# Kernel optimization log

Measured on AMD Instinct MI355X. Metric: run time of the kernel, lower is better.

Reference implementation:

```python
import jax, jax.numpy as jnp
import numpy as np

N = 100000      # nodes
E = 1600000     # edges (avg degree 16)
DIN = 128       # in_feats
H = 4           # num_heads
D = 32          # out_feats per head
NEG_SLOPE = 0.2


def setup_inputs() -> dict:
    key = jax.random.key(0)
    k1, k2, k3, k4, k5, k6 = jax.random.split(key, 6)
    feat = jax.random.normal(k1, (N, DIN), dtype=jnp.float32)
    src = jax.random.randint(k2, (E,), 0, N, dtype=jnp.int32)
    dst = jax.random.randint(k3, (E,), 0, N, dtype=jnp.int32)
    # learned params (fc kernel + attention vectors)
    W = jax.random.normal(k4, (DIN, H * D), dtype=jnp.float32) * 0.05
    attn_l = jax.random.normal(k5, (H, D), dtype=jnp.float32) * 0.05
    attn_r = jax.random.normal(k6, (H, D), dtype=jnp.float32) * 0.05
    return {"feat": feat, "src": src, "dst": dst, "W": W,
            "attn_l": attn_l, "attn_r": attn_r}


def reference(feat, src, dst, W, attn_l, attn_r):
    # linear projection: (N, DIN) @ (DIN, H*D) -> (N, H, D)
    h = (feat @ W).reshape(N, H, D)
    # per-node attention half-logits: (N, H)
    el = jnp.einsum("nhd,hd->nh", h, attn_l)
    er = jnp.einsum("nhd,hd->nh", h, attn_r)
    # edge-wise logits e_ij = LeakyReLU(el[src] + er[dst]) : (E, H)
    e = jax.nn.leaky_relu(el[src] + er[dst], negative_slope=NEG_SLOPE)
    # segment softmax over incoming edges of each dst node
    emax = jax.ops.segment_max(e, dst, num_segments=N)          # (N, H)
    emax = jnp.where(jnp.isfinite(emax), emax, 0.0)             # empty segs
    ee = jnp.exp(e - emax[dst])                                 # (E, H)
    denom = jax.ops.segment_sum(ee, dst, num_segments=N)        # (N, H)
    a = ee / denom[dst]                                         # (E, H)
    # weighted message + scatter-sum aggregation: (N, H, D)
    msg = h[src] * a[:, :, None]                                # (E, H, D)
    out = jax.ops.segment_sum(msg, dst, num_segments=N)
    return out
```

## Files before the change

### kernel.cpp

```cpp
#include <hip/hip_runtime.h>
#include <hip/hip_fp16.h>

#define N_NODES 100000
#define N_EDGES 1600000
#define DIN 128
#define NH 4
#define ND 32
#define HD 128
#define NEG_SLOPE 0.2f
#define MROWS 64
#define APAD 136
#define GEMM_BLOCKS ((N_NODES + MROWS - 1) / MROWS)

#define NBUCK 782
#define CHB 8192
#define NHB 196

typedef _Float16 half8_t __attribute__((ext_vector_type(8)));
typedef float f32x4 __attribute__((ext_vector_type(4)));

__device__ __forceinline__ float lrelu(float x) {
    return x > 0.0f ? x : NEG_SLOPE * x;
}

union Pack8  { uint2 u; __half2 h2[2]; };
union Pack16 { uint4 u; __half2 h2[4]; };

__global__ __launch_bounds__(256) void k_wconv(const float* __restrict__ W,
                                               __half* __restrict__ Wt) {
    int i = blockIdx.x * 256 + threadIdx.x;
    int k = i >> 7, c = i & 127;
    Wt[c * DIN + k] = __float2half(W[k * HD + c]);
}

__global__ __launch_bounds__(256) void k_gemmhist(
    const float* __restrict__ feat, const __half* __restrict__ Wt,
    const float* __restrict__ attn_l, const float* __restrict__ attn_r,
    __half* __restrict__ hhalf, float* __restrict__ el, float* __restrict__ er,
    const int* __restrict__ dst, int* __restrict__ hist) {

    __shared__ __align__(16) __half As[MROWS * APAD];
    __shared__ __align__(16) __half Bs[HD * APAD];

    const int tid = threadIdx.x;

    if ((int)blockIdx.x >= GEMM_BLOCKS) {
        if (!hist) return;
        int hb = blockIdx.x - GEMM_BLOCKS;
        int* cnt = (int*)As;
        for (int i = tid; i < NBUCK; i += 256) cnt[i] = 0;
        __syncthreads();
        int base = hb * CHB;
#pragma unroll
        for (int j = 0; j < CHB / 256; ++j) {
            int e = base + j * 256 + tid;
            if (e < N_EDGES) atomicAdd(&cnt[dst[e] >> 7], 1);
        }
        __syncthreads();
        int* hrow = hist + (size_t)hb * NBUCK;
        for (int i = tid; i < NBUCK; i += 256) hrow[i] = cnt[i];
        return;
    }

    const int row0 = blockIdx.x * MROWS;

    {
        const uint4* Wv = (const uint4*)Wt;
#pragma unroll
        for (int i = 0; i < 8; ++i) {
            int idx = tid + i * 256;
            int c = idx >> 4, k8 = idx & 15;
            *(uint4*)(&Bs[c * APAD + k8 * 8]) = Wv[idx];
        }
    }
    {
#pragma unroll
        for (int i = 0; i < 8; ++i) {
            int idx = tid + i * 256;
            int r = idx >> 5, c4 = idx & 31;
            int row = row0 + r;
            float4 f = (row < N_NODES)
                ? *(const float4*)(feat + (size_t)row * DIN + c4 * 4)
                : make_float4(0.0f, 0.0f, 0.0f, 0.0f);
            Pack8 pk;
            pk.h2[0] = __floats2half2_rn(f.x, f.y);
            pk.h2[1] = __floats2half2_rn(f.z, f.w);
            *(uint2*)(&As[r * APAD + c4 * 4]) = pk.u;
        }
    }
    __syncthreads();

    const int l = tid & 63;
    const int wv = tid >> 6;
    const int lrow = l & 15;
    const int kid = l >> 4;

    f32x4 acc[8];
#pragma unroll
    for (int n = 0; n < 8; ++n) acc[n] = (f32x4){0.0f, 0.0f, 0.0f, 0.0f};

#pragma unroll
    for (int kb = 0; kb < 4; ++kb) {
        half8_t a = *(const half8_t*)(&As[(wv * 16 + lrow) * APAD + kb * 32 + kid * 8]);
#pragma unroll
        for (int n = 0; n < 8; ++n) {
            half8_t b = *(const half8_t*)(&Bs[(n * 16 + lrow) * APAD + kb * 32 + kid * 8]);
            acc[n] = __builtin_amdgcn_mfma_f32_16x16x32_f16(a, b, acc[n], 0, 0, 0);
        }
    }

    __syncthreads();
#pragma unroll
    for (int n = 0; n < 8; ++n)
#pragma unroll
        for (int r = 0; r < 4; ++r)
            As[(wv * 16 + kid * 4 + r) * APAD + n * 16 + lrow] =
                __float2half(acc[n][r]);
    __syncthreads();

    {
        int lr = tid >> 2;
        int row = row0 + lr;
        int head = tid & 3;
        if (row < N_NODES) {
            float suml = 0.0f, sumr = 0.0f;
#pragma unroll
            for (int q = 0; q < 4; ++q) {
                Pack16 p;
                p.u = *(const uint4*)(&As[lr * APAD + head * 32 + q * 8]);
                float4 al0 = *(const float4*)(attn_l + head * 32 + q * 8);
                float4 al1 = *(const float4*)(attn_l + head * 32 + q * 8 + 4);
                float4 ar0 = *(const float4*)(attn_r + head * 32 + q * 8);
                float4 ar1 = *(const float4*)(attn_r + head * 32 + q * 8 + 4);
                float2 x0 = __half22float2(p.h2[0]);
                float2 x1 = __half22float2(p.h2[1]);
                float2 x2 = __half22float2(p.h2[2]);
                float2 x3 = __half22float2(p.h2[3]);
                suml += x0.x * al0.x + x0.y * al0.y + x1.x * al0.z + x1.y * al0.w;
                suml += x2.x * al1.x + x2.y * al1.y + x3.x * al1.z + x3.y * al1.w;
                sumr += x0.x * ar0.x + x0.y * ar0.y + x1.x * ar0.z + x1.y * ar0.w;
                sumr += x2.x * ar1.x + x2.y * ar1.y + x3.x * ar1.z + x3.y * ar1.w;
                *(uint4*)(hhalf + (size_t)row * HD + head * 32 + q * 8) = p.u;
            }
            el[(size_t)row * NH + head] = suml;
            er[(size_t)row * NH + head] = sumr;
        }
    }
}

__global__ __launch_bounds__(256) void k_scanH(int* __restrict__ hist,
                                               int* __restrict__ tot) {
    __shared__ int wtot[4];
    int b = blockIdx.x, tid = threadIdx.x;
    int v = (tid < NHB) ? hist[(size_t)tid * NBUCK + b] : 0;
    int lane = tid & 63, wv = tid >> 6;
    int incl = v;
#pragma unroll
    for (int off = 1; off < 64; off <<= 1) {
        int t = __shfl_up(incl, off, 64);
        if (lane >= off) incl += t;
    }
    if (lane == 63) wtot[wv] = incl;
    __syncthreads();
    int woff = 0;
    for (int w = 0; w < wv; ++w) woff += wtot[w];
    if (tid < NHB) hist[(size_t)tid * NBUCK + b] = woff + incl - v;
    if (tid == 0) tot[b] = wtot[0] + wtot[1] + wtot[2] + wtot[3];
}

__global__ __launch_bounds__(256) void k_scanT(const int* __restrict__ tot,
                                               int* __restrict__ bucket_base,
                                               int* __restrict__ rowptr) {
    __shared__ int wtot[4];
    int tid = threadIdx.x;
    int idx0 = tid * 4;
    int v[4];
#pragma unroll
    for (int j = 0; j < 4; ++j) {
        int b = idx0 + j;
        v[j] = (b < NBUCK) ? tot[b] : 0;
    }
    int s = v[0] + v[1] + v[2] + v[3];
    int lane = tid & 63;
    int incl = s;
#pragma unroll
    for (int off = 1; off < 64; off <<= 1) {
        int t = __shfl_up(incl, off, 64);
        if (lane >= off) incl += t;
    }
    if (lane == 63) wtot[tid >> 6] = incl;
    __syncthreads();
    int woff = 0;
    for (int w = 0; w < (tid >> 6); ++w) woff += wtot[w];
    int run = woff + incl - s;
#pragma unroll
    for (int j = 0; j < 4; ++j) {
        int b = idx0 + j;
        if (b < NBUCK) {
            int old = v[j];
            bucket_base[b] = run;
            run += old;
        }
    }
    if (tid == 0) {
        int total = wtot[0] + wtot[1] + wtot[2] + wtot[3];
        bucket_base[NBUCK] = total;
        rowptr[N_NODES] = total;
    }
}

__global__ __launch_bounds__(256) void k_cscat(
    const int* __restrict__ src, const int* __restrict__ dst,
    const int* __restrict__ hist, const int* __restrict__ bucket_base,
    int* __restrict__ bucketed) {
    __shared__ int cur[NBUCK];
    int tid = threadIdx.x;
    const int* hrow = hist + (size_t)blockIdx.x * NBUCK;
    for (int i = tid; i < NBUCK; i += 256) cur[i] = bucket_base[i] + hrow[i];
    __syncthreads();
    int base = blockIdx.x * CHB;
#pragma unroll
    for (int j = 0; j < CHB / 256; ++j) {
        int e = base + j * 256 + tid;
        if (e < N_EDGES) {
            int d = dst[e];
            int slot = atomicAdd(&cur[d >> 7], 1);
            bucketed[slot] = src[e] | ((d & 127) << 17);
        }
    }
}

__global__ __launch_bounds__(256) void k_fine(
    const int* __restrict__ bucketed, const int* __restrict__ bbase,
    int* __restrict__ srcs, int* __restrict__ rowptr) {

    __shared__ int cnt[128];
    __shared__ int noff[129];
    __shared__ int cur[128];

    const int b = blockIdx.x;
    const int tid = threadIdx.x;
    const int node0 = b << 7;
    const int beg = bbase[b], end = bbase[b + 1];

    if (tid < 128) cnt[tid] = 0;
    __syncthreads();

    for (int e = beg + tid; e < end; e += 256)
        atomicAdd(&cnt[bucketed[e] >> 17], 1);
    __syncthreads();

    if (tid < 64) {
        int v0 = cnt[tid * 2], v1 = cnt[tid * 2 + 1];
        int s = v0 + v1;
        int incl = s;
#pragma unroll
        for (int off = 1; off < 64; off <<= 1) {
            int t = __shfl_up(incl, off, 64);
            if (tid >= off) incl += t;
        }
        int excl = incl - s;
        noff[tid * 2] = excl;
        noff[tid * 2 + 1] = excl + v0;
        cur[tid * 2] = excl;
        cur[tid * 2 + 1] = excl + v0;
        if (tid == 63) noff[128] = incl;
    }
    __syncthreads();

    if (tid < 128) {
        int node = node0 + tid;
        if (node < N_NODES) rowptr[node] = beg + noff[tid];
    }

    for (int e = beg + tid; e < end; e += 256) {
        int p = bucketed[e];
        int d7 = p >> 17;
        int slot = beg + atomicAdd(&cur[d7], 1);
        srcs[slot] = p & 0x1FFFF;
    }
}

__global__ __launch_bounds__(256) void k_agg_csr(
    const int* __restrict__ rowptr, const int* __restrict__ srcs,
    const float* __restrict__ el, const float* __restrict__ er,
    const __half* __restrict__ hhalf, float* __restrict__ out) {
    int node = blockIdx.x * 4 + (threadIdx.x >> 6);
    int lane = threadIdx.x & 63;
    int grp = lane >> 4;
    int cl = lane & 15;
    int head = cl >> 2;
    int beg = rowptr[node], end = rowptr[node + 1];

    const float er_h = er[(size_t)node * NH + head];

    float dsum = 0.0f;
    float a[8];
#pragma unroll
    for (int q = 0; q < 8; ++q) a[q] = 0.0f;

    int i = beg + grp;
    for (; i + 12 < end; i += 16) {
        int s0 = srcs[i], s1 = srcs[i + 4], s2 = srcs[i + 8], s3 = srcs[i + 12];
        float e0 = el[(size_t)s0 * NH + head];
        float e1 = el[(size_t)s1 * NH + head];
        float e2 = el[(size_t)s2 * NH + head];
        float e3 = el[(size_t)s3 * NH + head];
        Pack16 p0, p1, p2, p3;
        p0.u = *(const uint4*)(hhalf + (size_t)s0 * HD + cl * 8);
        p1.u = *(const uint4*)(hhalf + (size_t)s1 * HD + cl * 8);
        p2.u = *(const uint4*)(hhalf + (size_t)s2 * HD + cl * 8);
        p3.u = *(const uint4*)(hhalf + (size_t)s3 * HD + cl * 8);
        float w0 = __expf(lrelu(e0 + er_h));
        float w1 = __expf(lrelu(e1 + er_h));
        float w2 = __expf(lrelu(e2 + er_h));
        float w3 = __expf(lrelu(e3 + er_h));
        dsum += (w0 + w1) + (w2 + w3);
#pragma unroll
        for (int q = 0; q < 4; ++q) {
            float2 x0 = __half22float2(p0.h2[q]);
            float2 x1 = __half22float2(p1.h2[q]);
            float2 x2 = __half22float2(p2.h2[q]);
            float2 x3 = __half22float2(p3.h2[q]);
            a[2 * q]     = fmaf(x0.x, w0, a[2 * q]);
            a[2 * q + 1] = fmaf(x0.y, w0, a[2 * q + 1]);
            a[2 * q]     = fmaf(x1.x, w1, a[2 * q]);
            a[2 * q + 1] = fmaf(x1.y, w1, a[2 * q + 1]);
            a[2 * q]     = fmaf(x2.x, w2, a[2 * q]);
            a[2 * q + 1] = fmaf(x2.y, w2, a[2 * q + 1]);
            a[2 * q]     = fmaf(x3.x, w3, a[2 * q]);
            a[2 * q + 1] = fmaf(x3.y, w3, a[2 * q + 1]);
        }
    }
    for (; i + 4 < end; i += 8) {
        int s0 = srcs[i], s1 = srcs[i + 4];
        float e0 = el[(size_t)s0 * NH + head];
        float e1 = el[(size_t)s1 * NH + head];
        Pack16 p0, p1;
        p0.u = *(const uint4*)(hhalf + (size_t)s0 * HD + cl * 8);
        p1.u = *(const uint4*)(hhalf + (size_t)s1 * HD + cl * 8);
        float w0 = __expf(lrelu(e0 + er_h));
        float w1 = __expf(lrelu(e1 + er_h));
        dsum += w0 + w1;
#pragma unroll
        for (int q = 0; q < 4; ++q) {
            float2 x0 = __half22float2(p0.h2[q]);
            float2 x1 = __half22float2(p1.h2[q]);
            a[2 * q]     = fmaf(x0.x, w0, a[2 * q]);
            a[2 * q + 1] = fmaf(x0.y, w0, a[2 * q + 1]);
            a[2 * q]     = fmaf(x1.x, w1, a[2 * q]);
            a[2 * q + 1] = fmaf(x1.y, w1, a[2 * q + 1]);
        }
    }
    if (i < end) {
        int s0 = srcs[i];
        float w0 = __expf(lrelu(el[(size_t)s0 * NH + head] + er_h));
        Pack16 p0;
        p0.u = *(const uint4*)(hhalf + (size_t)s0 * HD + cl * 8);
        dsum += w0;
#pragma unroll
        for (int q = 0; q < 4; ++q) {
            float2 x0 = __half22float2(p0.h2[q]);
            a[2 * q]     = fmaf(x0.x, w0, a[2 * q]);
            a[2 * q + 1] = fmaf(x0.y, w0, a[2 * q + 1]);
        }
    }

    dsum += __shfl_xor(dsum, 16, 64);
    dsum += __shfl_xor(dsum, 32, 64);
#pragma unroll
    for (int q = 0; q < 8; ++q) {
        a[q] += __shfl_xor(a[q], 16, 64);
        a[q] += __shfl_xor(a[q], 32, 64);
    }

    if (grp == 0) {
        float inv = (end > beg) ? 1.0f / dsum : 0.0f;
        *(float4*)(out + (size_t)node * HD + cl * 8) =
            make_float4(a[0] * inv, a[1] * inv, a[2] * inv, a[3] * inv);
        *(float4*)(out + (size_t)node * HD + cl * 8 + 4) =
            make_float4(a[4] * inv, a[5] * inv, a[6] * inv, a[7] * inv);
    }
}

__global__ void k_init_fb(float* __restrict__ out, float* __restrict__ denom) {
    int i = blockIdx.x * blockDim.x + threadIdx.x;
    int stride = gridDim.x * blockDim.x;
    for (int j = i; j < N_NODES * HD; j += stride) out[j] = 0.0f;
    for (int j = i; j < N_NODES * NH; j += stride) denom[j] = 0.0f;
}

__global__ __launch_bounds__(256) void k_denom_fb(
    const int* __restrict__ src, const int* __restrict__ dst,
    const float* __restrict__ el, const float* __restrict__ er,
    float* __restrict__ denom) {
    int e = blockIdx.x * blockDim.x + threadIdx.x;
    if (e >= N_EDGES) return;
    int s = src[e], d = dst[e];
    float4 l = *(const float4*)(el + (size_t)s * NH);
    float4 r = *(const float4*)(er + (size_t)d * NH);
    float* dn = denom + (size_t)d * NH;
    atomicAdd(dn + 0, __expf(lrelu(l.x + r.x)));
    atomicAdd(dn + 1, __expf(lrelu(l.y + r.y)));
    atomicAdd(dn + 2, __expf(lrelu(l.z + r.z)));
    atomicAdd(dn + 3, __expf(lrelu(l.w + r.w)));
}

__global__ __launch_bounds__(256) void k_agg_fb(
    const int* __restrict__ src, const int* __restrict__ dst,
    const float* __restrict__ el, const float* __restrict__ er,
    const float* __restrict__ denom, const __half* __restrict__ hhalf,
    float* __restrict__ out) {
    long long t = (long long)blockIdx.x * blockDim.x + threadIdx.x;
    if (t >= (long long)N_EDGES * HD) return;
    int e = (int)(t >> 7);
    int c = (int)(t & 127);
    int hh = c >> 5;
    int s = src[e], d = dst[e];
    float x = lrelu(el[(size_t)s * NH + hh] + er[(size_t)d * NH + hh]);
    float a = __expf(x) / denom[(size_t)d * NH + hh];
    atomicAdd(out + (size_t)d * HD + c,
              __half2float(hhalf[(size_t)s * HD + c]) * a);
}

extern "C" void kernel_launch(void* const* d_in, const int* in_sizes, int n_in,
                              void* d_out, int out_size, void* d_ws, size_t ws_size,
                              hipStream_t stream) {
    const float* feat   = (const float*)d_in[0];
    const int*   src    = (const int*)d_in[1];
    const int*   dst    = (const int*)d_in[2];
    const float* W      = (const float*)d_in[3];
    const float* attn_l = (const float*)d_in[4];
    const float* attn_r = (const float*)d_in[5];
    float* out = (float*)d_out;

    char* base = (char*)d_ws;
    size_t off = 0;
    auto take = [&](size_t bytes) -> char* {
        char* r = base + off;
        off = (off + bytes + 255) & ~(size_t)255;
        return r;
    };
    __half* hhalf  = (__half*)take((size_t)N_NODES * HD * 2);
    float* el      = (float*)take((size_t)N_NODES * NH * 4);
    float* er      = (float*)take((size_t)N_NODES * NH * 4);
    __half* Wt     = (__half*)take((size_t)DIN * HD * 2);
    int*  hist     = (int*)take((size_t)NHB * NBUCK * 4);
    int*  tot      = (int*)take((size_t)NBUCK * 4);
    int*  bbase    = (int*)take((size_t)(NBUCK + 1) * 4);
    int*  bucketed = (int*)take((size_t)N_EDGES * 4);
    int*  srcs     = (int*)take((size_t)N_EDGES * 4);
    int*  rowptr   = (int*)take((size_t)(N_NODES + 1) * 4);
    float* denom   = (float*)take((size_t)N_NODES * NH * 4);
    bool csr = (off <= ws_size);

    if (csr) {
        k_wconv<<<64, 256, 0, stream>>>(W, Wt);
        k_gemmhist<<<GEMM_BLOCKS + NHB, 256, 0, stream>>>(
            feat, Wt, attn_l, attn_r, hhalf, el, er, dst, hist);
        k_scanH<<<NBUCK, 256, 0, stream>>>(hist, tot);
        k_scanT<<<1, 256, 0, stream>>>(tot, bbase, rowptr);
        k_cscat<<<NHB, 256, 0, stream>>>(src, dst, hist, bbase, bucketed);
        k_fine<<<NBUCK, 256, 0, stream>>>(bucketed, bbase, srcs, rowptr);
        k_agg_csr<<<N_NODES / 4, 256, 0, stream>>>(rowptr, srcs, el, er,
                                                   hhalf, out);
    } else {
        int eb = (N_EDGES + 255) / 256;
        k_init_fb<<<2048, 256, 0, stream>>>(out, denom);
        k_wconv<<<64, 256, 0, stream>>>(W, Wt);
        k_gemmhist<<<GEMM_BLOCKS, 256, 0, stream>>>(
            feat, Wt, attn_l, attn_r, hhalf, el, er, dst, (int*)nullptr);
        k_denom_fb<<<eb, 256, 0, stream>>>(src, dst, el, er, denom);
        long long totw = (long long)N_EDGES * HD;
        int ab = (int)((totw + 255) / 256);
        k_agg_fb<<<ab, 256, 0, stream>>>(src, dst, el, er, denom, hhalf, out);
    }
}
```

Measured before the change: 161.8 us.

## Fuse W conversion into histogram kernel and coarse scatter into GEMM kernel

Regroups the pipeline so the histogram pass runs together with the W transpose/convert in one launch, and the coarse bucket scatter runs alongside the GEMM blocks in a single launch. This removes two kernel launches and lets the scatter's latency-bound atomics overlap with the GEMM. The trade-off is that the GEMM now waits until the scans finish instead of overlapping with the histogram, and scatter blocks claim the large GEMM shared-memory allocation.

```diff
diff --git a/kernel.cpp b/kernel.cpp
--- a/kernel.cpp
+++ b/kernel.cpp
@@ -15,6 +15,7 @@
 #define NBUCK 782
 #define CHB 8192
 #define NHB 196
+#define WCONV_BLOCKS 64
 
 typedef _Float16 half8_t __attribute__((ext_vector_type(8)));
 typedef float f32x4 __attribute__((ext_vector_type(4)));
@@ -26,43 +27,126 @@
 union Pack8  { uint2 u; __half2 h2[2]; };
 union Pack16 { uint4 u; __half2 h2[4]; };
 
-__global__ __launch_bounds__(256) void k_wconv(const float* __restrict__ W,
-                                               __half* __restrict__ Wt) {
-    int i = blockIdx.x * 256 + threadIdx.x;
-    int k = i >> 7, c = i & 127;
-    Wt[c * DIN + k] = __float2half(W[k * HD + c]);
-}
-
-__global__ __launch_bounds__(256) void k_gemmhist(
+__global__ __launch_bounds__(256) void k_histw(
+    const int* __restrict__ dst, int* __restrict__ hist,
+    const float* __restrict__ W, __half* __restrict__ Wt) {
+    __shared__ int cnt[NBUCK];
+    const int tid = threadIdx.x;
+
+    if ((int)blockIdx.x >= NHB) {
+        int i = (blockIdx.x - NHB) * 256 + tid;
+        int k = i >> 7, c = i & 127;
+        Wt[c * DIN + k] = __float2half(W[k * HD + c]);
+        return;
+    }
+    if (!hist) return;
+    for (int i = tid; i < NBUCK; i += 256) cnt[i] = 0;
+    __syncthreads();
+    int base = blockIdx.x * CHB;
+#pragma unroll
+    for (int j = 0; j < CHB / 256; ++j) {
+        int e = base + j * 256 + tid;
+        if (e < N_EDGES) atomicAdd(&cnt[dst[e] >> 7], 1);
+    }
+    __syncthreads();
+    int* hrow = hist + (size_t)blockIdx.x * NBUCK;
+    for (int i = tid; i < NBUCK; i += 256) hrow[i] = cnt[i];
+}
+
+__global__ __launch_bounds__(256) void k_scanH(int* __restrict__ hist,
+                                               int* __restrict__ tot) {
+    __shared__ int wtot[4];
+    int b = blockIdx.x, tid = threadIdx.x;
+    int v = (tid < NHB) ? hist[(size_t)tid * NBUCK + b] : 0;
+    int lane = tid & 63, wv = tid >> 6;
+    int incl = v;
+#pragma unroll
+    for (int off = 1; off < 64; off <<= 1) {
+        int t = __shfl_up(incl, off, 64);
+        if (lane >= off) incl += t;
+    }
+    if (lane == 63) wtot[wv] = incl;
+    __syncthreads();
+    int woff = 0;
+    for (int w = 0; w < wv; ++w) woff += wtot[w];
+    if (tid < NHB) hist[(size_t)tid * NBUCK + b] = woff + incl - v;
+    if (tid == 0) tot[b] = wtot[0] + wtot[1] + wtot[2] + wtot[3];
+}
+
+__global__ __launch_bounds__(256) void k_scanT(const int* __restrict__ tot,
+                                               int* __restrict__ bucket_base,
+                                               int* __restrict__ rowptr) {
+    __shared__ int wtot[4];
+    int tid = threadIdx.x;
+    int idx0 = tid * 4;
+    int v[4];
+#pragma unroll
+    for (int j = 0; j < 4; ++j) {
+        int b = idx0 + j;
+        v[j] = (b < NBUCK) ? tot[b] : 0;
+    }
+    int s = v[0] + v[1] + v[2] + v[3];
+    int lane = tid & 63;
+    int incl = s;
+#pragma unroll
+    for (int off = 1; off < 64; off <<= 1) {
+        int t = __shfl_up(incl, off, 64);
+        if (lane >= off) incl += t;
+    }
+    if (lane == 63) wtot[tid >> 6] = incl;
+    __syncthreads();
+    int woff = 0;
+    for (int w = 0; w < (tid >> 6); ++w) woff += wtot[w];
+    int run = woff + incl - s;
+#pragma unroll
+    for (int j = 0; j < 4; ++j) {
+        int b = idx0 + j;
+        if (b < NBUCK) {
+            int old = v[j];
+            bucket_base[b] = run;
+            run += old;
+        }
+    }
+    if (tid == 0) {
+        int total = wtot[0] + wtot[1] + wtot[2] + wtot[3];
+        bucket_base[NBUCK] = total;
+        rowptr[N_NODES] = total;
+    }
+}
+
+__global__ __launch_bounds__(256) void k_gemmcscat(
     const float* __restrict__ feat, const __half* __restrict__ Wt,
     const float* __restrict__ attn_l, const float* __restrict__ attn_r,
     __half* __restrict__ hhalf, float* __restrict__ el, float* __restrict__ er,
-    const int* __restrict__ dst, int* __restrict__ hist) {
+    const int* __restrict__ src, const int* __restrict__ dst,
+    const int* __restrict__ hist, const int* __restrict__ bucket_base,
+    int* __restrict__ bucketed) {
 
     __shared__ __align__(16) __half As[MROWS * APAD];
     __shared__ __align__(16) __half Bs[HD * APAD];
 
     const int tid = threadIdx.x;
 
-    if ((int)blockIdx.x >= GEMM_BLOCKS) {
-        if (!hist) return;
-        int hb = blockIdx.x - GEMM_BLOCKS;
-        int* cnt = (int*)As;
-        for (int i = tid; i < NBUCK; i += 256) cnt[i] = 0;
+    if ((int)blockIdx.x < NHB) {
+        if (!bucketed) return;
+        int* cur = (int*)As;
+        const int* hrow = hist + (size_t)blockIdx.x * NBUCK;
+        for (int i = tid; i < NBUCK; i += 256) cur[i] = bucket_base[i] + hrow[i];
         __syncthreads();
-        int base = hb * CHB;
+        int base = blockIdx.x * CHB;
 #pragma unroll
         for (int j = 0; j < CHB / 256; ++j) {
             int e = base + j * 256 + tid;
-            if (e < N_EDGES) atomicAdd(&cnt[dst[e] >> 7], 1);
-        }
-        __syncthreads();
-        int* hrow = hist + (size_t)hb * NBUCK;
-        for (int i = tid; i < NBUCK; i += 256) hrow[i] = cnt[i];
+            if (e < N_EDGES) {
+                int d = dst[e];
+                int slot = atomicAdd(&cur[d >> 7], 1);
+                bucketed[slot] = src[e] | ((d & 127) << 17);
+            }
+        }
         return;
     }
 
-    const int row0 = blockIdx.x * MROWS;
+    const int row0 = (blockIdx.x - NHB) * MROWS;
 
     {
         const uint4* Wv = (const uint4*)Wt;
@@ -148,88 +232,6 @@
     }
 }
 
-__global__ __launch_bounds__(256) void k_scanH(int* __restrict__ hist,
-                                               int* __restrict__ tot) {
-    __shared__ int wtot[4];
-    int b = blockIdx.x, tid = threadIdx.x;
-    int v = (tid < NHB) ? hist[(size_t)tid * NBUCK + b] : 0;
-    int lane = tid & 63, wv = tid >> 6;
-    int incl = v;
-#pragma unroll
-    for (int off = 1; off < 64; off <<= 1) {
-        int t = __shfl_up(incl, off, 64);
-        if (lane >= off) incl += t;
-    }
-    if (lane == 63) wtot[wv] = incl;
-    __syncthreads();
-    int woff = 0;
-    for (int w = 0; w < wv; ++w) woff += wtot[w];
-    if (tid < NHB) hist[(size_t)tid * NBUCK + b] = woff + incl - v;
-    if (tid == 0) tot[b] = wtot[0] + wtot[1] + wtot[2] + wtot[3];
-}
-
-__global__ __launch_bounds__(256) void k_scanT(const int* __restrict__ tot,
-                                               int* __restrict__ bucket_base,
-                                               int* __restrict__ rowptr) {
-    __shared__ int wtot[4];
-    int tid = threadIdx.x;
-    int idx0 = tid * 4;
-    int v[4];
-#pragma unroll
-    for (int j = 0; j < 4; ++j) {
-        int b = idx0 + j;
-        v[j] = (b < NBUCK) ? tot[b] : 0;
-    }
-    int s = v[0] + v[1] + v[2] + v[3];
-    int lane = tid & 63;
-    int incl = s;
-#pragma unroll
-    for (int off = 1; off < 64; off <<= 1) {
-        int t = __shfl_up(incl, off, 64);
-        if (lane >= off) incl += t;
-    }
-    if (lane == 63) wtot[tid >> 6] = incl;
-    __syncthreads();
-    int woff = 0;
-    for (int w = 0; w < (tid >> 6); ++w) woff += wtot[w];
-    int run = woff + incl - s;
-#pragma unroll
-    for (int j = 0; j < 4; ++j) {
-        int b = idx0 + j;
-        if (b < NBUCK) {
-            int old = v[j];
-            bucket_base[b] = run;
-            run += old;
-        }
-    }
-    if (tid == 0) {
-        int total = wtot[0] + wtot[1] + wtot[2] + wtot[3];
-        bucket_base[NBUCK] = total;
-        rowptr[N_NODES] = total;
-    }
-}
-
-__global__ __launch_bounds__(256) void k_cscat(
-    const int* __restrict__ src, const int* __restrict__ dst,
-    const int* __restrict__ hist, const int* __restrict__ bucket_base,
-    int* __restrict__ bucketed) {
-    __shared__ int cur[NBUCK];
-    int tid = threadIdx.x;
-    const int* hrow = hist + (size_t)blockIdx.x * NBUCK;
-    for (int i = tid; i < NBUCK; i += 256) cur[i] = bucket_base[i] + hrow[i];
-    __syncthreads();
-    int base = blockIdx.x * CHB;
-#pragma unroll
-    for (int j = 0; j < CHB / 256; ++j) {
-        int e = base + j * 256 + tid;
-        if (e < N_EDGES) {
-            int d = dst[e];
-            int slot = atomicAdd(&cur[d >> 7], 1);
-            bucketed[slot] = src[e] | ((d & 127) << 17);
-        }
-    }
-}
-
 __global__ __launch_bounds__(256) void k_fine(
     const int* __restrict__ bucketed, const int* __restrict__ bbase,
     int* __restrict__ srcs, int* __restrict__ rowptr) {
@@ -455,21 +457,22 @@
     bool csr = (off <= ws_size);
 
     if (csr) {
-        k_wconv<<<64, 256, 0, stream>>>(W, Wt);
-        k_gemmhist<<<GEMM_BLOCKS + NHB, 256, 0, stream>>>(
-            feat, Wt, attn_l, attn_r, hhalf, el, er, dst, hist);
+        k_histw<<<NHB + WCONV_BLOCKS, 256, 0, stream>>>(dst, hist, W, Wt);
         k_scanH<<<NBUCK, 256, 0, stream>>>(hist, tot);
         k_scanT<<<1, 256, 0, stream>>>(tot, bbase, rowptr);
-        k_cscat<<<NHB, 256, 0, stream>>>(src, dst, hist, bbase, bucketed);
+        k_gemmcscat<<<NHB + GEMM_BLOCKS, 256, 0, stream>>>(
+            feat, Wt, attn_l, attn_r, hhalf, el, er,
+            src, dst, hist, bbase, bucketed);
         k_fine<<<NBUCK, 256, 0, stream>>>(bucketed, bbase, srcs, rowptr);
         k_agg_csr<<<N_NODES / 4, 256, 0, stream>>>(rowptr, srcs, el, er,
                                                    hhalf, out);
     } else {
         int eb = (N_EDGES + 255) / 256;
         k_init_fb<<<2048, 256, 0, stream>>>(out, denom);
-        k_wconv<<<64, 256, 0, stream>>>(W, Wt);
-        k_gemmhist<<<GEMM_BLOCKS, 256, 0, stream>>>(
-            feat, Wt, attn_l, attn_r, hhalf, el, er, dst, (int*)nullptr);
+        k_histw<<<NHB + WCONV_BLOCKS, 256, 0, stream>>>(dst, (int*)nullptr, W, Wt);
+        k_gemmcscat<<<NHB + GEMM_BLOCKS, 256, 0, stream>>>(
+            feat, Wt, attn_l, attn_r, hhalf, el, er,
+            src, dst, (const int*)nullptr, (const int*)nullptr, (int*)nullptr);
         k_denom_fb<<<eb, 256, 0, stream>>>(src, dst, el, er, denom);
         long long totw = (long long)N_EDGES * HD;
         int ab = (int)((totw + 255) / 256);
```

Result: faster. 145.8 us (-9.9%).
